# Kernel optimization log

Measured on AMD Instinct MI355X. Metric: run time of the kernel, lower is better.

## Reference

```python
import jax, jax.numpy as jnp
import numpy as np
from jax import lax

T, B, S = 64, 32, 64
V, E, H = 32000, 512, 512

def _p(key, shape, scale=0.05):
    return (jax.random.normal(key, shape, dtype=jnp.float32) * scale)

def setup_inputs() -> dict:
    key = jax.random.key(0)
    ks = jax.random.split(key, 24)
    inp = {
        'trg': jax.random.randint(ks[0], (T, B), 0, V),
        'encoded_src': jax.random.normal(ks[1], (S, B, 2 * H), dtype=jnp.float32),
        'emb': _p(ks[2], (V, E)),
        # LSTM layer 0: input = E + 2H
        'W_ih0': _p(ks[3], (4 * H, E + 2 * H)), 'W_hh0': _p(ks[4], (4 * H, H)),
        'b_ih0': _p(ks[5], (4 * H,)), 'b_hh0': _p(ks[6], (4 * H,)),
        # LSTM layer 1: input = H
        'W_ih1': _p(ks[7], (4 * H, H)), 'W_hh1': _p(ks[8], (4 * H, H)),
        'b_ih1': _p(ks[9], (4 * H,)), 'b_hh1': _p(ks[10], (4 * H,)),
        # attn_annot: 2H -> H
        'Wa': _p(ks[11], (H, 2 * H)), 'ba': _p(ks[12], (H,)),
        # attn_hidden: H -> H
        'Wh': _p(ks[13], (H, H)), 'bh': _p(ks[14], (H,)),
        # other: H -> 1
        'Wo': _p(ks[15], (1, H)), 'bo': _p(ks[16], (1,)),
        # penult: 3H -> E
        'Wp': _p(ks[17], (E, 3 * H)), 'bp': _p(ks[18], (E,)),
        # out bias (weight tied to emb)
        'b_out': _p(ks[19], (V,)),
    }
    return inp

def _lstm_cell(x, h, c, W_ih, W_hh, b_ih, b_hh):
    # PyTorch gate order: i, f, g, o
    g = x @ W_ih.T + b_ih + h @ W_hh.T + b_hh
    i, f, gg, o = jnp.split(g, 4, axis=-1)
    c_new = jax.nn.sigmoid(f) * c + jax.nn.sigmoid(i) * jnp.tanh(gg)
    h_new = jax.nn.sigmoid(o) * jnp.tanh(c_new)
    return h_new, c_new

def reference(trg, encoded_src, emb, W_ih0, W_hh0, b_ih0, b_hh0,
              W_ih1, W_hh1, b_ih1, b_hh1, Wa, ba, Wh, bh, Wo, bo,
              Wp, bp, b_out):
    trg_emb = emb[trg]                                # [T,B,E]
    annot_scores = encoded_src @ Wa.T + ba            # [S,B,H]
    Hd = W_hh0.shape[1]
    Bd = encoded_src.shape[1]
    h0 = jnp.zeros((2, Bd, Hd), dtype=encoded_src.dtype)
    c0 = jnp.zeros((2, Bd, Hd), dtype=encoded_src.dtype)
    ctx0 = jnp.zeros((Bd, encoded_src.shape[2]), dtype=encoded_src.dtype)

    def step(carry, emb_t):
        h, c, ctx = carry
        x = jnp.concatenate([emb_t, ctx], axis=1)      # [B, E+2H]
        h0n, c0n = _lstm_cell(x,   h[0], c[0], W_ih0, W_hh0, b_ih0, b_hh0)
        h1n, c1n = _lstm_cell(h0n, h[1], c[1], W_ih1, W_hh1, b_ih1, b_hh1)
        out = h1n                                      # [B,H]
        hs = out @ Wh.T + bh                           # [B,H]
        e = jnp.tanh(hs[None] + annot_scores) @ Wo.T + bo   # [S,B,1]
        a = jax.nn.softmax(e, axis=0)[..., 0]          # [S,B]
        ctx_new = jnp.einsum('sb,sbd->bd', a, encoded_src)  # [B,2H]
        stacked = jnp.concatenate([out, ctx_new], axis=1)   # [B,3H]
        return (jnp.stack([h0n, h1n]), jnp.stack([c0n, c1n]), ctx_new), stacked

    (h, c, _), all_scores = lax.scan(step, (h0, c0, ctx0), trg_emb)  # all_scores [T,B,3H]
    pen = all_scores @ Wp.T + bp                       # [T,B,E]
    logits = pen @ emb.T + b_out                       # [T,B,V] (tied weights)
    scores = jax.nn.log_softmax(logits, axis=2)
    return (scores, h, c)
```

## Files before the change

kernel.cpp:

```cpp
#include <hip/hip_runtime.h>


typedef unsigned short u16;
typedef short bf16x8 __attribute__((ext_vector_type(8)));
typedef float f32x4 __attribute__((ext_vector_type(4)));

#define MFMA_BF16(a, b, c) __builtin_amdgcn_mfma_f32_16x16x32_bf16((a), (b), (c), 0, 0, 0)

struct __attribute__((aligned(8))) U16x4 { u16 x, y, z, w; };

__device__ __forceinline__ float b2f(u16 u) {
  unsigned v = ((unsigned)u) << 16; float f; __builtin_memcpy(&f, &v, 4); return f;
}
__device__ __forceinline__ u16 f2b(float f) {
  unsigned u; __builtin_memcpy(&u, &f, 4);
  u = (u + 0x7FFFu + ((u >> 16) & 1u)) >> 16;
  return (u16)u;
}
__device__ __forceinline__ float sigm(float x) { return 1.f / (1.f + __expf(-x)); }
__device__ __forceinline__ float tanh_fast(float x) {
  x = fminf(fmaxf(x, -15.f), 15.f);
  float e = __expf(2.f * x);
  return (e - 1.f) / (e + 1.f);
}

__device__ __forceinline__ bf16x8 bl16(const u16* p) {
  bf16x8 v;
  asm volatile("global_load_dwordx4 %0, %1, off sc0 sc1" : "=v"(v) : "v"(p) : "memory");
  return v;
}
__device__ __forceinline__ float blf(const float* p) {
  float v;
  asm volatile("global_load_dword %0, %1, off sc0 sc1" : "=v"(v) : "v"(p) : "memory");
  return v;
}
__device__ __forceinline__ u16 blu16(const u16* p) {
  unsigned v;
  asm volatile("global_load_ushort %0, %1, off sc0 sc1" : "=v"(v) : "v"(p) : "memory");
  return (u16)v;
}
__device__ __forceinline__ void bs16(u16* p, u16 d) {
  unsigned dd = d;
  asm volatile("global_store_short %0, %1, off sc0 sc1" :: "v"(p), "v"(dd) : "memory");
}
__device__ __forceinline__ void bs32(float* p, float d) {
  asm volatile("global_store_dword %0, %1, off sc0 sc1" :: "v"(p), "v"(d) : "memory");
}
__device__ __forceinline__ void bs32u(u16* p, unsigned d) {
  asm volatile("global_store_dword %0, %1, off sc0 sc1" :: "v"(p), "v"(d) : "memory");
}
__device__ __forceinline__ void vmwait() {
  asm volatile("s_waitcnt vmcnt(0)" ::: "memory");
  __builtin_amdgcn_sched_barrier(0);
}

__global__ void f2b4_kernel(const float* __restrict__ src, u16* __restrict__ dst, long n4) {
  long i = (long)blockIdx.x * blockDim.x + threadIdx.x;
  long stride = (long)gridDim.x * blockDim.x;
  for (; i < n4; i += stride) {
    float4 v = ((const float4*)src)[i];
    U16x4 o; o.x = f2b(v.x); o.y = f2b(v.y); o.z = f2b(v.z); o.w = f2b(v.w);
    ((U16x4*)dst)[i] = o;
  }
}

__global__ void f2b4_strided(const float* __restrict__ src, u16* __restrict__ dst,
                             int rows, int cols4, int sld, int soff, int dld, int doff) {
  int total = rows * cols4;
  for (int i = blockIdx.x * blockDim.x + threadIdx.x; i < total; i += gridDim.x * blockDim.x) {
    int r = i / cols4, c4 = i - r * cols4;
    float4 v = *(const float4*)(src + (size_t)r * sld + soff + c4 * 4);
    U16x4 o; o.x = f2b(v.x); o.y = f2b(v.y); o.z = f2b(v.z); o.w = f2b(v.w);
    *(U16x4*)(dst + (size_t)r * dld + doff + c4 * 4) = o;
  }
}

__global__ void gather_emb_kernel(const int* __restrict__ trg, const float* __restrict__ emb,
                                  u16* __restrict__ out) {
  int r = blockIdx.x;
  int v = trg[r];
  const float* srow = emb + (size_t)v * 512;
  u16* drow = out + (size_t)r * 512;
  for (int e = threadIdx.x; e < 128; e += blockDim.x) {
    float4 x = ((const float4*)srow)[e];
    U16x4 o; o.x = f2b(x.x); o.y = f2b(x.y); o.z = f2b(x.z); o.w = f2b(x.w);
    ((U16x4*)drow)[e] = o;
  }
}

__global__ void annot_tr_kernel(const float* __restrict__ annot, u16* __restrict__ abt) {
  int b = blockIdx.x >> 6, s = blockIdx.x & 63;
  const float* src = annot + (size_t)(s * 32 + b) * 512;
  u16* dst = abt + (size_t)(b * 64 + s) * 512;
  int j = threadIdx.x;
  float4 v = ((const float4*)src)[j];
  U16x4 o; o.x = f2b(v.x); o.y = f2b(v.y); o.z = f2b(v.z); o.w = f2b(v.w);
  ((U16x4*)dst)[j] = o;
}

__global__ void enc_tr_kernel(const float* __restrict__ enc, u16* __restrict__ ebt) {
  int b = blockIdx.x >> 6, s = blockIdx.x & 63;
  const float* src = enc + (size_t)(s * 32 + b) * 1024;
  u16* dst = ebt + (size_t)(b * 64 + s) * 1024;
  int j = threadIdx.x;
  float4 v = ((const float4*)src)[j];
  U16x4 o; o.x = f2b(v.x); o.y = f2b(v.y); o.z = f2b(v.z); o.w = f2b(v.w);
  ((U16x4*)dst)[j] = o;
}

template <int MODE>
__global__ __launch_bounds__(256) void gemm_bt(
    const u16* __restrict__ A, const u16* __restrict__ B,
    float* __restrict__ outF, u16* __restrict__ outB,
    const float* __restrict__ bias0, const float* __restrict__ bias1,
    int N, int K, int ntiles, float* __restrict__ pmax, float* __restrict__ psum) {
  const int l = threadIdx.x & 63, wv = threadIdx.x >> 6;
  const int m0 = blockIdx.x * 128 + wv * 32;
  const int n0 = blockIdx.y * 64;
  const int kg = ((l >> 4) << 3);
  const u16* Ap0 = A + (size_t)(m0 + (l & 15)) * K + kg;
  const u16* Ap1 = Ap0 + (size_t)16 * K;
  const u16* Bp = B + (size_t)(n0 + (l & 15)) * K + kg;
  f32x4 acc[2][4] = {};
  for (int k0 = 0; k0 < K; k0 += 32) {
    bf16x8 a0 = *(const bf16x8*)(Ap0 + k0);
    bf16x8 a1 = *(const bf16x8*)(Ap1 + k0);
#pragma unroll
    for (int nf = 0; nf < 4; ++nf) {
      bf16x8 bb = *(const bf16x8*)(Bp + (size_t)(nf * 16) * K + k0);
      acc[0][nf] = MFMA_BF16(a0, bb, acc[0][nf]);
      acc[1][nf] = MFMA_BF16(a1, bb, acc[1][nf]);
    }
  }
  float biasv[4];
#pragma unroll
  for (int nf = 0; nf < 4; ++nf) {
    int col = n0 + nf * 16 + (l & 15);
    float bv = bias0 ? bias0[col] : 0.f;
    if (bias1) bv += bias1[col];
    biasv[nf] = bv;
  }
#pragma unroll
  for (int mi = 0; mi < 2; ++mi)
#pragma unroll
    for (int nf = 0; nf < 4; ++nf)
#pragma unroll
      for (int i = 0; i < 4; ++i) acc[mi][nf][i] += biasv[nf];

#pragma unroll
  for (int mi = 0; mi < 2; ++mi)
#pragma unroll
    for (int i = 0; i < 4; ++i) {
      int row = m0 + mi * 16 + ((l >> 4) << 2) + i;
#pragma unroll
      for (int nf = 0; nf < 4; ++nf) {
        int col = n0 + nf * 16 + (l & 15);
        if constexpr (MODE == 1)
          outB[(size_t)row * N + col] = f2b(acc[mi][nf][i]);
        else
          outF[(size_t)row * N + col] = acc[mi][nf][i];
      }
    }
  if constexpr (MODE == 2) {
    float lm[2][4], se[2][4];
#pragma unroll
    for (int mi = 0; mi < 2; ++mi)
#pragma unroll
      for (int i = 0; i < 4; ++i) {
        float m_ = acc[mi][0][i];
#pragma unroll
        for (int nf = 1; nf < 4; ++nf) m_ = fmaxf(m_, acc[mi][nf][i]);
        lm[mi][i] = m_;
      }
#pragma unroll
    for (int d = 1; d < 16; d <<= 1)
#pragma unroll
      for (int mi = 0; mi < 2; ++mi)
#pragma unroll
        for (int i = 0; i < 4; ++i) lm[mi][i] = fmaxf(lm[mi][i], __shfl_xor(lm[mi][i], d));
#pragma unroll
    for (int mi = 0; mi < 2; ++mi)
#pragma unroll
      for (int i = 0; i < 4; ++i) {
        float s_ = 0.f;
#pragma unroll
        for (int nf = 0; nf < 4; ++nf) s_ += __expf(acc[mi][nf][i] - lm[mi][i]);
        se[mi][i] = s_;
      }
#pragma unroll
    for (int d = 1; d < 16; d <<= 1)
#pragma unroll
      for (int mi = 0; mi < 2; ++mi)
#pragma unroll
        for (int i = 0; i < 4; ++i) se[mi][i] += __shfl_xor(se[mi][i], d);
    if ((l & 15) == 0) {
#pragma unroll
      for (int mi = 0; mi < 2; ++mi)
#pragma unroll
        for (int i = 0; i < 4; ++i) {
          int row = m0 + mi * 16 + ((l >> 4) << 2) + i;
          pmax[(size_t)row * ntiles + blockIdx.y] = lm[mi][i];
          psum[(size_t)row * ntiles + blockIdx.y] = se[mi][i];
        }
    }
  }
}

__device__ __forceinline__ void grid_barrier(unsigned* flags, unsigned phase) {
  __syncthreads();
  if (threadIdx.x == 0) {
    __hip_atomic_store(flags + blockIdx.x * 32, phase, __ATOMIC_RELAXED,
                       __HIP_MEMORY_SCOPE_AGENT);
  }
  if (threadIdx.x < 32) {
    int spins = 0;
    while (__hip_atomic_load(flags + threadIdx.x * 32, __ATOMIC_RELAXED,
                             __HIP_MEMORY_SCOPE_AGENT) < phase &&
           spins < 2000000) ++spins;
  }
  __syncthreads();
}

__global__ __launch_bounds__(512, 2) void scan_kernel(
    const u16* __restrict__ xW0,
    const u16* __restrict__ Wcat0,
    const u16* __restrict__ Wcat1,
    const u16* __restrict__ Whb,
    const float* __restrict__ b_ih1, const float* __restrict__ b_hh1,
    const float* __restrict__ bh, const float* __restrict__ Wo, const float* __restrict__ bo,
    const u16* __restrict__ annot_bt,
    const u16* __restrict__ enc_bt,
    u16* __restrict__ ctxb,
    u16* __restrict__ h0b,
    u16* __restrict__ h1b,
    float* __restrict__ c0, float* __restrict__ c1,
    float* __restrict__ hs,
    u16* __restrict__ scoresb,
    float* __restrict__ dout_hc,
    unsigned* __restrict__ flags) {
  __shared__ float sm[16384];
  const int w = blockIdx.x;
  const int tid = threadIdx.x;
  const int l = tid & 63, wv = tid >> 6;
  const int jh0 = w * 16;
  const int bE = tid >> 4, jlE = tid & 15;
  unsigned phase = 0;

  float gb1[4];
#pragma unroll
  for (int g = 0; g < 4; ++g) gb1[g] = b_ih1[g * 512 + jh0 + jlE] + b_hh1[g * 512 + jh0 + jlE];
  const float bhv = bh[jh0 + jlE];
  const float bov = bo[0];

  for (int t = 0; t < 64; ++t) {
    const int pA = t & 1;
    {
      const int kg = ((l >> 4) << 3);
      u16 xw[4];
      {
        const u16* xp = xW0 + (size_t)(t * 32 + bE) * 2048 + jh0 + jlE;
#pragma unroll
        for (int g = 0; g < 4; ++g) xw[g] = blu16(xp + g * 512);
      }
      bf16x8 a0[6], a1[6];
#pragma unroll
      for (int kk = 0; kk < 6; ++kk) {
        const int k0 = wv * 192 + kk * 32;
        const u16* ab; int ld, off;
        if (k0 < 1024) { ab = ctxb; ld = 1024; off = k0; }
        else { ab = h0b + pA * 32 * 512; ld = 512; off = k0 - 1024; }
        a0[kk] = bl16(ab + (size_t)(l & 15) * ld + off + kg);
        a1[kk] = bl16(ab + (size_t)((l & 15) + 16) * ld + off + kg);
      }
      vmwait();
      f32x4 acc[2][4] = {};
#pragma unroll
      for (int kk = 0; kk < 6; ++kk) {
        const int k0 = wv * 192 + kk * 32;
#pragma unroll
        for (int g = 0; g < 4; ++g) {
          bf16x8 bb = *(const bf16x8*)(Wcat0 + (size_t)(g * 512 + jh0 + (l & 15)) * 1536 + k0 + kg);
          acc[0][g] = MFMA_BF16(a0[kk], bb, acc[0][g]);
          acc[1][g] = MFMA_BF16(a1[kk], bb, acc[1][g]);
        }
      }
#pragma unroll
      for (int mi = 0; mi < 2; ++mi)
#pragma unroll
        for (int g = 0; g < 4; ++g)
#pragma unroll
          for (int i = 0; i < 4; ++i) {
            int m = mi * 16 + ((l >> 4) << 2) + i;
            sm[(wv * 32 + m) * 64 + g * 16 + (l & 15)] = acc[mi][g][i];
          }
      __syncthreads();
      {
        const int b = bE, jl = jlE, jh = jh0 + jl;
        float gate[4];
#pragma unroll
        for (int g = 0; g < 4; ++g) {
          float s = 0.f;
#pragma unroll
          for (int kv = 0; kv < 8; ++kv) s += sm[(kv * 32 + b) * 64 + g * 16 + jl];
          gate[g] = s + b2f(xw[g]);
        }
        float cn = sigm(gate[1]) * c0[b * 512 + jh] + sigm(gate[0]) * tanh_fast(gate[2]);
        float hn = sigm(gate[3]) * tanh_fast(cn);
        c0[b * 512 + jh] = cn;
        bs16(h0b + (pA ^ 1) * 32 * 512 + b * 512 + jh, f2b(hn));
        if (t == 63) { dout_hc[b * 512 + jh] = hn; dout_hc[32768 + b * 512 + jh] = cn; }
      }
    }
    grid_barrier(flags, ++phase);
    {
      const int kg = ((l >> 4) << 3);
      bf16x8 a0[4], a1[4];
#pragma unroll
      for (int kk = 0; kk < 4; ++kk) {
        const int k0 = wv * 128 + kk * 32;
        const u16* ab; int off;
        if (k0 < 512) { ab = h0b + (pA ^ 1) * 32 * 512; off = k0; }
        else { ab = h1b + pA * 32 * 512; off = k0 - 512; }
        a0[kk] = bl16(ab + (size_t)(l & 15) * 512 + off + kg);
        a1[kk] = bl16(ab + (size_t)((l & 15) + 16) * 512 + off + kg);
      }
      vmwait();
      f32x4 acc[2][4] = {};
#pragma unroll
      for (int kk = 0; kk < 4; ++kk) {
        const int k0 = wv * 128 + kk * 32;
#pragma unroll
        for (int g = 0; g < 4; ++g) {
          bf16x8 bb = *(const bf16x8*)(Wcat1 + (size_t)(g * 512 + jh0 + (l & 15)) * 1024 + k0 + kg);
          acc[0][g] = MFMA_BF16(a0[kk], bb, acc[0][g]);
          acc[1][g] = MFMA_BF16(a1[kk], bb, acc[1][g]);
        }
      }
#pragma unroll
      for (int mi = 0; mi < 2; ++mi)
#pragma unroll
        for (int g = 0; g < 4; ++g)
#pragma unroll
          for (int i = 0; i < 4; ++i) {
            int m = mi * 16 + ((l >> 4) << 2) + i;
            sm[(wv * 32 + m) * 64 + g * 16 + (l & 15)] = acc[mi][g][i];
          }
      __syncthreads();
      {
        const int b = bE, jl = jlE, jh = jh0 + jl;
        float gate[4];
#pragma unroll
        for (int g = 0; g < 4; ++g) {
          float s = 0.f;
#pragma unroll
          for (int kv = 0; kv < 8; ++kv) s += sm[(kv * 32 + b) * 64 + g * 16 + jl];
          gate[g] = s + gb1[g];
        }
        float cn = sigm(gate[1]) * c1[b * 512 + jh] + sigm(gate[0]) * tanh_fast(gate[2]);
        float hn = sigm(gate[3]) * tanh_fast(cn);
        c1[b * 512 + jh] = cn;
        u16 hb = f2b(hn);
        bs16(h1b + (pA ^ 1) * 32 * 512 + b * 512 + jh, hb);
        bs16(scoresb + (size_t)(t * 32 + b) * 1536 + jh, hb);
        if (t == 63) { dout_hc[16384 + b * 512 + jh] = hn; dout_hc[32768 + 16384 + b * 512 + jh] = cn; }
      }
    }
    grid_barrier(flags, ++phase);
    {
      const int kg = ((l >> 4) << 3);
      const u16* h1n = h1b + (pA ^ 1) * 32 * 512;
      bf16x8 a0[2], a1[2];
#pragma unroll
      for (int kk = 0; kk < 2; ++kk) {
        const int k0 = wv * 64 + kk * 32;
        a0[kk] = bl16(h1n + (size_t)(l & 15) * 512 + k0 + kg);
        a1[kk] = bl16(h1n + (size_t)((l & 15) + 16) * 512 + k0 + kg);
      }
      vmwait();
      f32x4 acc2[2] = {};
#pragma unroll
      for (int kk = 0; kk < 2; ++kk) {
        const int k0 = wv * 64 + kk * 32;
        bf16x8 bb = *(const bf16x8*)(Whb + (size_t)(jh0 + (l & 15)) * 512 + k0 + kg);
        acc2[0] = MFMA_BF16(a0[kk], bb, acc2[0]);
        acc2[1] = MFMA_BF16(a1[kk], bb, acc2[1]);
      }
#pragma unroll
      for (int mi = 0; mi < 2; ++mi)
#pragma unroll
        for (int i = 0; i < 4; ++i)
          sm[(wv * 32 + mi * 16 + ((l >> 4) << 2) + i) * 16 + (l & 15)] = acc2[mi][i];
      __syncthreads();
      {
        const int b = bE, jl = jlE;
        float s = 0.f;
#pragma unroll
        for (int kv = 0; kv < 8; ++kv) s += sm[(kv * 32 + b) * 16 + jl];
        bs32(hs + b * 512 + jh0 + jl, s + bhv);
      }
    }
    grid_barrier(flags, ++phase);
    {
      const int b = w;
      float* hs_s = sm;
      float* wo_s = sm + 512;
      float* red = sm + 1024;
      float* a_s = sm + 1536;
      float hv = blf(hs + b * 512 + tid);
      float wov = Wo[tid];
      vmwait();
      hs_s[tid] = hv;
      wo_s[tid] = wov;
      __syncthreads();
      const int s_ = tid >> 3, ks = tid & 7;
      const u16* arow = annot_bt + (size_t)(b * 64 + s_) * 512 + ks * 64;
      float accv = 0.f;
#pragma unroll
      for (int kk8 = 0; kk8 < 8; ++kk8) {
        bf16x8 av = *(const bf16x8*)(arow + kk8 * 8);
#pragma unroll
        for (int j = 0; j < 8; ++j) {
          int k = ks * 64 + kk8 * 8 + j;
          accv += tanh_fast(hs_s[k] + b2f((u16)av[j])) * wo_s[k];
        }
      }
      red[tid] = accv;
      __syncthreads();
      if (tid < 64) {
        float e = bov;
#pragma unroll
        for (int j = 0; j < 8; ++j) e += red[tid * 8 + j];
        float mx = e;
#pragma unroll
        for (int d = 1; d < 64; d <<= 1) mx = fmaxf(mx, __shfl_xor(mx, d));
        float p = __expf(e - mx);
        float ss = p;
#pragma unroll
        for (int d = 1; d < 64; d <<= 1) ss += __shfl_xor(ss, d);
        a_s[tid] = p / ss;
      }
      __syncthreads();
      float cx0 = 0.f, cx1 = 0.f;
      const u16* erow = enc_bt + (size_t)b * 65536 + tid * 2;
#pragma unroll 8
      for (int s2 = 0; s2 < 64; ++s2) {
        unsigned ev = *(const unsigned*)(erow + (size_t)s2 * 1024);
        float av = a_s[s2];
        cx0 += av * b2f((u16)(ev & 0xFFFFu));
        cx1 += av * b2f((u16)(ev >> 16));
      }
      u16 u0 = f2b(cx0), u1 = f2b(cx1);
      unsigned pk = (unsigned)u0 | ((unsigned)u1 << 16);
      bs32u(ctxb + b * 1024 + tid * 2, pk);
      bs32u(scoresb + (size_t)(t * 32 + b) * 1536 + 512 + tid * 2, pk);
    }
    grid_barrier(flags, ++phase);
  }
}

__global__ __launch_bounds__(256) void lse_kernel(const float* __restrict__ pmax,
                                                  const float* __restrict__ psum,
                                                  float* __restrict__ lse, int nt) {
  __shared__ float red[256];
  const int r = blockIdx.x;
  float m = -3.4e38f;
  for (int j = threadIdx.x; j < nt; j += 256) m = fmaxf(m, pmax[(size_t)r * nt + j]);
  red[threadIdx.x] = m; __syncthreads();
  for (int s = 128; s > 0; s >>= 1) {
    if (threadIdx.x < s) red[threadIdx.x] = fmaxf(red[threadIdx.x], red[threadIdx.x + s]);
    __syncthreads();
  }
  const float M = red[0]; __syncthreads();
  float s_ = 0.f;
  for (int j = threadIdx.x; j < nt; j += 256)
    s_ += psum[(size_t)r * nt + j] * __expf(pmax[(size_t)r * nt + j] - M);
  red[threadIdx.x] = s_; __syncthreads();
  for (int s = 128; s > 0; s >>= 1) {
    if (threadIdx.x < s) red[threadIdx.x] += red[threadIdx.x + s];
    __syncthreads();
  }
  if (threadIdx.x == 0) lse[r] = M + logf(red[0]);
}

__global__ void finalize_kernel(float* __restrict__ out, const float* __restrict__ lse) {
  const long n4 = 16384000;
  for (long i = (long)blockIdx.x * blockDim.x + threadIdx.x; i < n4;
       i += (long)gridDim.x * blockDim.x) {
    float4 v = ((float4*)out)[i];
    float L = lse[i / 8000];
    v.x -= L; v.y -= L; v.z -= L; v.w -= L;
    ((float4*)out)[i] = v;
  }
}

extern "C" void kernel_launch(void* const* d_in, const int* in_sizes, int n_in,
                              void* d_out, int out_size, void* d_ws, size_t ws_size,
                              hipStream_t stream) {
  const int* trg = (const int*)d_in[0];
  const float* enc = (const float*)d_in[1];
  const float* emb = (const float*)d_in[2];
  const float* W_ih0 = (const float*)d_in[3];
  const float* W_hh0 = (const float*)d_in[4];
  const float* b_ih0 = (const float*)d_in[5];
  const float* b_hh0 = (const float*)d_in[6];
  const float* W_ih1 = (const float*)d_in[7];
  const float* W_hh1 = (const float*)d_in[8];
  const float* b_ih1 = (const float*)d_in[9];
  const float* b_hh1 = (const float*)d_in[10];
  const float* Wa = (const float*)d_in[11];
  const float* ba = (const float*)d_in[12];
  const float* Wh = (const float*)d_in[13];
  const float* bh = (const float*)d_in[14];
  const float* Wo = (const float*)d_in[15];
  const float* bo = (const float*)d_in[16];
  const float* Wp = (const float*)d_in[17];
  const float* bp = (const float*)d_in[18];
  const float* b_out = (const float*)d_in[19];
  float* out = (float*)d_out;

  unsigned char* ws = (unsigned char*)d_ws;
  size_t off = 0;
  auto alloc = [&](size_t bytes) -> void* {
    void* p = ws + off; off += (bytes + 255) & ~(size_t)255; return p;
  };
  u16* emb_b = (u16*)alloc(32768000);
  u16* trgemb_b = (u16*)alloc(2097152);
  u16* enc_b = (u16*)alloc(4194304);
  u16* Wemb0_b = (u16*)alloc(2097152);
  u16* Wcat0_b = (u16*)alloc(6291456);
  u16* Wcat1_b = (u16*)alloc(4194304);
  u16* Wa_b = (u16*)alloc(1048576);
  u16* Wh_b = (u16*)alloc(524288);
  u16* Wp_b = (u16*)alloc(1572864);
  u16* xW0_b = (u16*)alloc(8388608);
  float* annot = (float*)alloc(4194304);
  u16* scoresb = (u16*)alloc(6291456);
  u16* pen_b = (u16*)alloc(2097152);
  u16* ctxb = (u16*)alloc(65536);
  u16* h0b = (u16*)alloc(65536);
  u16* h1b = (u16*)alloc(65536);
  float* c0 = (float*)alloc(65536);
  float* c1 = (float*)alloc(65536);
  float* hsbuf = (float*)alloc(65536);
  float* pmax = (float*)alloc(4194304);
  float* psum = (float*)alloc(4194304);
  float* lse = (float*)alloc(8192);
  unsigned* flags = (unsigned*)alloc(4096);
  if (off > ws_size) return;

  u16* annot_bt = (u16*)pmax;
  u16* enc_bt = (u16*)psum;

  hipMemsetAsync(ctxb, 0, 65536, stream);
  hipMemsetAsync(h0b, 0, 65536, stream);
  hipMemsetAsync(h1b, 0, 65536, stream);
  hipMemsetAsync(c0, 0, 65536, stream);
  hipMemsetAsync(c1, 0, 65536, stream);
  hipMemsetAsync(flags, 0, 4096, stream);

  f2b4_kernel<<<1024, 256, 0, stream>>>(emb, emb_b, 4096000);
  f2b4_kernel<<<256, 256, 0, stream>>>(enc, enc_b, 524288);
  f2b4_kernel<<<128, 256, 0, stream>>>(Wa, Wa_b, 131072);
  f2b4_kernel<<<64, 256, 0, stream>>>(Wh, Wh_b, 65536);
  f2b4_kernel<<<128, 256, 0, stream>>>(Wp, Wp_b, 196608);
  f2b4_strided<<<512, 256, 0, stream>>>(W_ih0, Wemb0_b, 2048, 128, 1536, 0, 512, 0);
  f2b4_strided<<<512, 256, 0, stream>>>(W_ih0, Wcat0_b, 2048, 256, 1536, 512, 1536, 0);
  f2b4_strided<<<512, 256, 0, stream>>>(W_hh0, Wcat0_b, 2048, 128, 512, 0, 1536, 1024);
  f2b4_strided<<<512, 256, 0, stream>>>(W_ih1, Wcat1_b, 2048, 128, 512, 0, 1024, 0);
  f2b4_strided<<<512, 256, 0, stream>>>(W_hh1, Wcat1_b, 2048, 128, 512, 0, 1024, 512);
  gather_emb_kernel<<<2048, 128, 0, stream>>>(trg, emb, trgemb_b);
  enc_tr_kernel<<<2048, 256, 0, stream>>>(enc, enc_bt);

  gemm_bt<1><<<dim3(16, 32), 256, 0, stream>>>(trgemb_b, Wemb0_b, nullptr, xW0_b,
                                               b_ih0, b_hh0, 2048, 512, 0, nullptr, nullptr);
  gemm_bt<0><<<dim3(16, 8), 256, 0, stream>>>(enc_b, Wa_b, annot, nullptr,
                                              ba, nullptr, 512, 1024, 0, nullptr, nullptr);
  annot_tr_kernel<<<2048, 128, 0, stream>>>(annot, annot_bt);

  scan_kernel<<<32, 512, 0, stream>>>(xW0_b, Wcat0_b, Wcat1_b, Wh_b, b_ih1, b_hh1, bh, Wo, bo,
                                      annot_bt, enc_bt, ctxb, h0b, h1b, c0, c1, hsbuf, scoresb,
                                      out + 65536000, flags);
  gemm_bt<1><<<dim3(16, 8), 256, 0, stream>>>(scoresb, Wp_b, nullptr, pen_b,
                                              bp, nullptr, 512, 1536, 0, nullptr, nullptr);
  gemm_bt<2><<<dim3(16, 500), 256, 0, stream>>>(pen_b, emb_b, out, nullptr,
                                                b_out, nullptr, 32000, 512, 500, pmax, psum);
  lse_kernel<<<2048, 256, 0, stream>>>(pmax, psum, lse, 500);
  finalize_kernel<<<2048, 256, 0, stream>>>(out, lse);
}
```

Baseline: 2.522 ms.

## Overlap output projection and vocab GEMM with recurrent scan in a persistent mega-kernel

Merges the recurrent scan, the penultimate projection and the vocabulary logits GEMM into one persistent 224-block kernel. Every 7th block runs the serial LSTM/attention recurrence, and the remaining 192 blocks wait on the step flags and compute pen and logits for timestep t while the recurrence moves ahead. This hides the large tied-weight GEMM behind the latency-bound scan. In exchange it adds spin-waiting on flags, relies on all blocks being co-resident, and changes the vocab tile width and the partial max/sum layout to 250 tiles.

```diff
diff --git a/kernel.cpp b/kernel.cpp
--- a/kernel.cpp
+++ b/kernel.cpp
@@ -43,10 +43,10 @@
   unsigned dd = d;
   asm volatile("global_store_short %0, %1, off sc0 sc1" :: "v"(p), "v"(dd) : "memory");
 }
-__device__ __forceinline__ void bs32(float* p, float d) {
+__device__ __forceinline__ void bs32u(u16* p, unsigned d) {
   asm volatile("global_store_dword %0, %1, off sc0 sc1" :: "v"(p), "v"(d) : "memory");
 }
-__device__ __forceinline__ void bs32u(u16* p, unsigned d) {
+__device__ __forceinline__ void bsf32(float* p, float d) {
   asm volatile("global_store_dword %0, %1, off sc0 sc1" :: "v"(p), "v"(d) : "memory");
 }
 __device__ __forceinline__ void vmwait() {
@@ -113,7 +113,7 @@
     const u16* __restrict__ A, const u16* __restrict__ B,
     float* __restrict__ outF, u16* __restrict__ outB,
     const float* __restrict__ bias0, const float* __restrict__ bias1,
-    int N, int K, int ntiles, float* __restrict__ pmax, float* __restrict__ psum) {
+    int N, int K) {
   const int l = threadIdx.x & 63, wv = threadIdx.x >> 6;
   const int m0 = blockIdx.x * 128 + wv * 32;
   const int n0 = blockIdx.y * 64;
@@ -143,85 +143,36 @@
 #pragma unroll
   for (int mi = 0; mi < 2; ++mi)
 #pragma unroll
-    for (int nf = 0; nf < 4; ++nf)
-#pragma unroll
-      for (int i = 0; i < 4; ++i) acc[mi][nf][i] += biasv[nf];
-
-#pragma unroll
-  for (int mi = 0; mi < 2; ++mi)
-#pragma unroll
     for (int i = 0; i < 4; ++i) {
       int row = m0 + mi * 16 + ((l >> 4) << 2) + i;
 #pragma unroll
       for (int nf = 0; nf < 4; ++nf) {
         int col = n0 + nf * 16 + (l & 15);
+        float v = acc[mi][nf][i] + biasv[nf];
         if constexpr (MODE == 1)
-          outB[(size_t)row * N + col] = f2b(acc[mi][nf][i]);
+          outB[(size_t)row * N + col] = f2b(v);
         else
-          outF[(size_t)row * N + col] = acc[mi][nf][i];
+          outF[(size_t)row * N + col] = v;
       }
     }
-  if constexpr (MODE == 2) {
-    float lm[2][4], se[2][4];
-#pragma unroll
-    for (int mi = 0; mi < 2; ++mi)
-#pragma unroll
-      for (int i = 0; i < 4; ++i) {
-        float m_ = acc[mi][0][i];
-#pragma unroll
-        for (int nf = 1; nf < 4; ++nf) m_ = fmaxf(m_, acc[mi][nf][i]);
-        lm[mi][i] = m_;
-      }
-#pragma unroll
-    for (int d = 1; d < 16; d <<= 1)
-#pragma unroll
-      for (int mi = 0; mi < 2; ++mi)
-#pragma unroll
-        for (int i = 0; i < 4; ++i) lm[mi][i] = fmaxf(lm[mi][i], __shfl_xor(lm[mi][i], d));
-#pragma unroll
-    for (int mi = 0; mi < 2; ++mi)
-#pragma unroll
-      for (int i = 0; i < 4; ++i) {
-        float s_ = 0.f;
-#pragma unroll
-        for (int nf = 0; nf < 4; ++nf) s_ += __expf(acc[mi][nf][i] - lm[mi][i]);
-        se[mi][i] = s_;
-      }
-#pragma unroll
-    for (int d = 1; d < 16; d <<= 1)
-#pragma unroll
-      for (int mi = 0; mi < 2; ++mi)
-#pragma unroll
-        for (int i = 0; i < 4; ++i) se[mi][i] += __shfl_xor(se[mi][i], d);
-    if ((l & 15) == 0) {
-#pragma unroll
-      for (int mi = 0; mi < 2; ++mi)
-#pragma unroll
-        for (int i = 0; i < 4; ++i) {
-          int row = m0 + mi * 16 + ((l >> 4) << 2) + i;
-          pmax[(size_t)row * ntiles + blockIdx.y] = lm[mi][i];
-          psum[(size_t)row * ntiles + blockIdx.y] = se[mi][i];
-        }
-    }
-  }
-}
-
-__device__ __forceinline__ void grid_barrier(unsigned* flags, unsigned phase) {
+}
+
+__device__ __forceinline__ void grid_barrier(unsigned* flags, unsigned phase, int w) {
   __syncthreads();
   if (threadIdx.x == 0) {
-    __hip_atomic_store(flags + blockIdx.x * 32, phase, __ATOMIC_RELAXED,
+    __hip_atomic_store(flags + (size_t)w * 32, phase, __ATOMIC_RELAXED,
                        __HIP_MEMORY_SCOPE_AGENT);
   }
   if (threadIdx.x < 32) {
     int spins = 0;
-    while (__hip_atomic_load(flags + threadIdx.x * 32, __ATOMIC_RELAXED,
+    while (__hip_atomic_load(flags + (size_t)threadIdx.x * 32, __ATOMIC_RELAXED,
                              __HIP_MEMORY_SCOPE_AGENT) < phase &&
            spins < 2000000) ++spins;
   }
   __syncthreads();
 }
 
-__global__ __launch_bounds__(512, 2) void scan_kernel(
+__global__ __launch_bounds__(512, 2) void mega_kernel(
     const u16* __restrict__ xW0,
     const u16* __restrict__ Wcat0,
     const u16* __restrict__ Wcat1,
@@ -230,231 +181,375 @@
     const float* __restrict__ bh, const float* __restrict__ Wo, const float* __restrict__ bo,
     const u16* __restrict__ annot_bt,
     const u16* __restrict__ enc_bt,
-    u16* __restrict__ ctxb,
-    u16* __restrict__ h0b,
-    u16* __restrict__ h1b,
-    float* __restrict__ c0, float* __restrict__ c1,
-    float* __restrict__ hs,
-    u16* __restrict__ scoresb,
-    float* __restrict__ dout_hc,
-    unsigned* __restrict__ flags) {
+    u16* ctxb, u16* h0b, u16* h1b,
+    float* c0, float* c1,
+    float* hs,
+    u16* scoresb,
+    float* dout_hc,
+    unsigned* flags,
+    const u16* __restrict__ Wp,
+    const float* __restrict__ bp, const u16* __restrict__ emb_b,
+    const float* __restrict__ b_out,
+    u16* pen_b,
+    float* out, float* pmax, float* psum) {
   __shared__ float sm[16384];
-  const int w = blockIdx.x;
+  const int bx = blockIdx.x;
   const int tid = threadIdx.x;
   const int l = tid & 63, wv = tid >> 6;
-  const int jh0 = w * 16;
-  const int bE = tid >> 4, jlE = tid & 15;
-  unsigned phase = 0;
-
-  float gb1[4];
-#pragma unroll
-  for (int g = 0; g < 4; ++g) gb1[g] = b_ih1[g * 512 + jh0 + jlE] + b_hh1[g * 512 + jh0 + jlE];
-  const float bhv = bh[jh0 + jlE];
-  const float bov = bo[0];
-
-  for (int t = 0; t < 64; ++t) {
-    const int pA = t & 1;
-    {
-      const int kg = ((l >> 4) << 3);
-      u16 xw[4];
+
+  if (bx % 7 == 0) {
+    const int w = bx / 7;
+    const int jh0 = w * 16;
+    const int bE = tid >> 4, jlE = tid & 15;
+    unsigned phase = 0;
+
+    float gb1[4];
+#pragma unroll
+    for (int g = 0; g < 4; ++g) gb1[g] = b_ih1[g * 512 + jh0 + jlE] + b_hh1[g * 512 + jh0 + jlE];
+    const float bhv = bh[jh0 + jlE];
+    const float bov = bo[0];
+
+    for (int t = 0; t < 64; ++t) {
+      const int pA = t & 1;
       {
-        const u16* xp = xW0 + (size_t)(t * 32 + bE) * 2048 + jh0 + jlE;
-#pragma unroll
-        for (int g = 0; g < 4; ++g) xw[g] = blu16(xp + g * 512);
-      }
-      bf16x8 a0[6], a1[6];
-#pragma unroll
-      for (int kk = 0; kk < 6; ++kk) {
-        const int k0 = wv * 192 + kk * 32;
-        const u16* ab; int ld, off;
-        if (k0 < 1024) { ab = ctxb; ld = 1024; off = k0; }
-        else { ab = h0b + pA * 32 * 512; ld = 512; off = k0 - 1024; }
-        a0[kk] = bl16(ab + (size_t)(l & 15) * ld + off + kg);
-        a1[kk] = bl16(ab + (size_t)((l & 15) + 16) * ld + off + kg);
-      }
-      vmwait();
-      f32x4 acc[2][4] = {};
-#pragma unroll
-      for (int kk = 0; kk < 6; ++kk) {
-        const int k0 = wv * 192 + kk * 32;
-#pragma unroll
-        for (int g = 0; g < 4; ++g) {
-          bf16x8 bb = *(const bf16x8*)(Wcat0 + (size_t)(g * 512 + jh0 + (l & 15)) * 1536 + k0 + kg);
-          acc[0][g] = MFMA_BF16(a0[kk], bb, acc[0][g]);
-          acc[1][g] = MFMA_BF16(a1[kk], bb, acc[1][g]);
-        }
-      }
-#pragma unroll
-      for (int mi = 0; mi < 2; ++mi)
-#pragma unroll
-        for (int g = 0; g < 4; ++g)
+        const int kg = ((l >> 4) << 3);
+        u16 xw[4];
+        {
+          const u16* xp = xW0 + (size_t)(t * 32 + bE) * 2048 + jh0 + jlE;
+#pragma unroll
+          for (int g = 0; g < 4; ++g) xw[g] = blu16(xp + g * 512);
+        }
+        bf16x8 a0[6], a1[6];
+#pragma unroll
+        for (int kk = 0; kk < 6; ++kk) {
+          const int k0 = wv * 192 + kk * 32;
+          const u16* ab; int ld, off;
+          if (k0 < 1024) { ab = ctxb; ld = 1024; off = k0; }
+          else { ab = h0b + pA * 16384; ld = 512; off = k0 - 1024; }
+          a0[kk] = bl16(ab + (size_t)(l & 15) * ld + off + kg);
+          a1[kk] = bl16(ab + (size_t)((l & 15) + 16) * ld + off + kg);
+        }
+        vmwait();
+        f32x4 acc[2][4] = {};
+#pragma unroll
+        for (int kk = 0; kk < 6; ++kk) {
+          const int k0 = wv * 192 + kk * 32;
+#pragma unroll
+          for (int g = 0; g < 4; ++g) {
+            bf16x8 bb = *(const bf16x8*)(Wcat0 + (size_t)(g * 512 + jh0 + (l & 15)) * 1536 + k0 + kg);
+            acc[0][g] = MFMA_BF16(a0[kk], bb, acc[0][g]);
+            acc[1][g] = MFMA_BF16(a1[kk], bb, acc[1][g]);
+          }
+        }
+#pragma unroll
+        for (int mi = 0; mi < 2; ++mi)
+#pragma unroll
+          for (int g = 0; g < 4; ++g)
+#pragma unroll
+            for (int i = 0; i < 4; ++i) {
+              int m = mi * 16 + ((l >> 4) << 2) + i;
+              sm[(wv * 32 + m) * 64 + g * 16 + (l & 15)] = acc[mi][g][i];
+            }
+        __syncthreads();
+        {
+          const int b = bE, jl = jlE, jh = jh0 + jl;
+          float gate[4];
+#pragma unroll
+          for (int g = 0; g < 4; ++g) {
+            float s = 0.f;
+#pragma unroll
+            for (int kv = 0; kv < 8; ++kv) s += sm[(kv * 32 + b) * 64 + g * 16 + jl];
+            gate[g] = s + b2f(xw[g]);
+          }
+          float cn = sigm(gate[1]) * c0[b * 512 + jh] + sigm(gate[0]) * tanh_fast(gate[2]);
+          float hn = sigm(gate[3]) * tanh_fast(cn);
+          c0[b * 512 + jh] = cn;
+          bs16(h0b + (pA ^ 1) * 16384 + b * 512 + jh, f2b(hn));
+          if (t == 63) { dout_hc[b * 512 + jh] = hn; dout_hc[32768 + b * 512 + jh] = cn; }
+        }
+      }
+      grid_barrier(flags, ++phase, w);
+      {
+        const int kg = ((l >> 4) << 3);
+        bf16x8 a0[4], a1[4];
+#pragma unroll
+        for (int kk = 0; kk < 4; ++kk) {
+          const int k0 = wv * 128 + kk * 32;
+          const u16* ab; int off;
+          if (k0 < 512) { ab = h0b + (pA ^ 1) * 16384; off = k0; }
+          else { ab = h1b + pA * 16384; off = k0 - 512; }
+          a0[kk] = bl16(ab + (size_t)(l & 15) * 512 + off + kg);
+          a1[kk] = bl16(ab + (size_t)((l & 15) + 16) * 512 + off + kg);
+        }
+        vmwait();
+        f32x4 acc[2][4] = {};
+#pragma unroll
+        for (int kk = 0; kk < 4; ++kk) {
+          const int k0 = wv * 128 + kk * 32;
+#pragma unroll
+          for (int g = 0; g < 4; ++g) {
+            bf16x8 bb = *(const bf16x8*)(Wcat1 + (size_t)(g * 512 + jh0 + (l & 15)) * 1024 + k0 + kg);
+            acc[0][g] = MFMA_BF16(a0[kk], bb, acc[0][g]);
+            acc[1][g] = MFMA_BF16(a1[kk], bb, acc[1][g]);
+          }
+        }
+#pragma unroll
+        for (int mi = 0; mi < 2; ++mi)
+#pragma unroll
+          for (int g = 0; g < 4; ++g)
+#pragma unroll
+            for (int i = 0; i < 4; ++i) {
+              int m = mi * 16 + ((l >> 4) << 2) + i;
+              sm[(wv * 32 + m) * 64 + g * 16 + (l & 15)] = acc[mi][g][i];
+            }
+        __syncthreads();
+        {
+          const int b = bE, jl = jlE, jh = jh0 + jl;
+          float gate[4];
+#pragma unroll
+          for (int g = 0; g < 4; ++g) {
+            float s = 0.f;
+#pragma unroll
+            for (int kv = 0; kv < 8; ++kv) s += sm[(kv * 32 + b) * 64 + g * 16 + jl];
+            gate[g] = s + gb1[g];
+          }
+          float cn = sigm(gate[1]) * c1[b * 512 + jh] + sigm(gate[0]) * tanh_fast(gate[2]);
+          float hn = sigm(gate[3]) * tanh_fast(cn);
+          c1[b * 512 + jh] = cn;
+          u16 hb = f2b(hn);
+          bs16(h1b + (pA ^ 1) * 16384 + b * 512 + jh, hb);
+          bs16(scoresb + (size_t)(t * 32 + b) * 1536 + jh, hb);
+          if (t == 63) { dout_hc[16384 + b * 512 + jh] = hn; dout_hc[49152 + b * 512 + jh] = cn; }
+        }
+      }
+      grid_barrier(flags, ++phase, w);
+      {
+        const int kg = ((l >> 4) << 3);
+        const u16* h1n = h1b + (pA ^ 1) * 16384;
+        bf16x8 a0[2], a1[2];
+#pragma unroll
+        for (int kk = 0; kk < 2; ++kk) {
+          const int k0 = wv * 64 + kk * 32;
+          a0[kk] = bl16(h1n + (size_t)(l & 15) * 512 + k0 + kg);
+          a1[kk] = bl16(h1n + (size_t)((l & 15) + 16) * 512 + k0 + kg);
+        }
+        vmwait();
+        f32x4 acc2[2] = {};
+#pragma unroll
+        for (int kk = 0; kk < 2; ++kk) {
+          const int k0 = wv * 64 + kk * 32;
+          bf16x8 bb = *(const bf16x8*)(Whb + (size_t)(jh0 + (l & 15)) * 512 + k0 + kg);
+          acc2[0] = MFMA_BF16(a0[kk], bb, acc2[0]);
+          acc2[1] = MFMA_BF16(a1[kk], bb, acc2[1]);
+        }
+#pragma unroll
+        for (int mi = 0; mi < 2; ++mi)
+#pragma unroll
+          for (int i = 0; i < 4; ++i)
+            sm[(wv * 32 + mi * 16 + ((l >> 4) << 2) + i) * 16 + (l & 15)] = acc2[mi][i];
+        __syncthreads();
+        {
+          const int b = bE, jl = jlE;
+          float s = 0.f;
+#pragma unroll
+          for (int kv = 0; kv < 8; ++kv) s += sm[(kv * 32 + b) * 16 + jl];
+          bsf32(hs + b * 512 + jh0 + jl, s + bhv);
+        }
+      }
+      grid_barrier(flags, ++phase, w);
+      {
+        const int b = w;
+        float* hs_s = sm;
+        float* wo_s = sm + 512;
+        float* red = sm + 1024;
+        float* a_s = sm + 1536;
+        float hv = blf(hs + b * 512 + tid);
+        float wov = Wo[tid];
+        vmwait();
+        hs_s[tid] = hv;
+        wo_s[tid] = wov;
+        __syncthreads();
+        const int s_ = tid >> 3, ks = tid & 7;
+        const u16* arow = annot_bt + (size_t)(b * 64 + s_) * 512 + ks * 64;
+        float accv = 0.f;
+#pragma unroll
+        for (int kk8 = 0; kk8 < 8; ++kk8) {
+          bf16x8 av = *(const bf16x8*)(arow + kk8 * 8);
+#pragma unroll
+          for (int j = 0; j < 8; ++j) {
+            int k = ks * 64 + kk8 * 8 + j;
+            accv += tanh_fast(hs_s[k] + b2f((u16)av[j])) * wo_s[k];
+          }
+        }
+        red[tid] = accv;
+        __syncthreads();
+        if (tid < 64) {
+          float e = bov;
+#pragma unroll
+          for (int j = 0; j < 8; ++j) e += red[tid * 8 + j];
+          float mx = e;
+#pragma unroll
+          for (int d = 1; d < 64; d <<= 1) mx = fmaxf(mx, __shfl_xor(mx, d));
+          float p = __expf(e - mx);
+          float ss = p;
+#pragma unroll
+          for (int d = 1; d < 64; d <<= 1) ss += __shfl_xor(ss, d);
+          a_s[tid] = p / ss;
+        }
+        __syncthreads();
+        float cx0 = 0.f, cx1 = 0.f;
+        const u16* erow = enc_bt + (size_t)b * 65536 + tid * 2;
+#pragma unroll 8
+        for (int s2 = 0; s2 < 64; ++s2) {
+          unsigned ev = *(const unsigned*)(erow + (size_t)s2 * 1024);
+          float av = a_s[s2];
+          cx0 += av * b2f((u16)(ev & 0xFFFFu));
+          cx1 += av * b2f((u16)(ev >> 16));
+        }
+        unsigned pk = (unsigned)f2b(cx0) | ((unsigned)f2b(cx1) << 16);
+        bs32u(ctxb + b * 1024 + tid * 2, pk);
+        bs32u(scoresb + (size_t)(t * 32 + b) * 1536 + 512 + tid * 2, pk);
+      }
+      grid_barrier(flags, ++phase, w);
+    }
+  } else {
+    const int wid = bx - bx / 7 - 1;
+    const int kg = (l >> 4) << 3;
+    const int tile1 = wid, tile2 = 192 + wid;
+    const int ntile = (tile2 < 250) ? 2 : 1;
+
+    for (int t = 0; t < 64; ++t) {
+      if (tid < 32) {
+        int spins = 0;
+        while (__hip_atomic_load(flags + (size_t)tid * 32, __ATOMIC_RELAXED,
+                                 __HIP_MEMORY_SCOPE_AGENT) < (unsigned)(4 * (t + 1)) &&
+               spins < 8000000) { __builtin_amdgcn_s_sleep(2); ++spins; }
+      }
+      __syncthreads();
+
+      if (wid == (t % 192)) {
+        const u16* Ap0 = scoresb + (size_t)(t * 32 + (l & 15)) * 1536 + kg;
+        const u16* Ap1 = Ap0 + (size_t)16 * 1536;
+        const int cv = wv * 64;
+        const u16* Bp = Wp + (size_t)(cv + (l & 15)) * 1536 + kg;
+        f32x4 acc[2][4] = {};
+        for (int kc = 0; kc < 1536; kc += 128) {
+          bf16x8 bfr[4][4];
+#pragma unroll
+          for (int kk = 0; kk < 4; ++kk)
+#pragma unroll
+            for (int nf = 0; nf < 4; ++nf)
+              bfr[kk][nf] = bl16(Bp + (size_t)(nf * 16) * 1536 + kc + kk * 32);
+          vmwait();
+#pragma unroll
+          for (int kk = 0; kk < 4; ++kk) {
+            bf16x8 a0 = *(const bf16x8*)(Ap0 + kc + kk * 32);
+            bf16x8 a1 = *(const bf16x8*)(Ap1 + kc + kk * 32);
+#pragma unroll
+            for (int nf = 0; nf < 4; ++nf) {
+              acc[0][nf] = MFMA_BF16(a0, bfr[kk][nf], acc[0][nf]);
+              acc[1][nf] = MFMA_BF16(a1, bfr[kk][nf], acc[1][nf]);
+            }
+          }
+        }
+#pragma unroll
+        for (int mi = 0; mi < 2; ++mi)
 #pragma unroll
           for (int i = 0; i < 4; ++i) {
-            int m = mi * 16 + ((l >> 4) << 2) + i;
-            sm[(wv * 32 + m) * 64 + g * 16 + (l & 15)] = acc[mi][g][i];
-          }
+            int row = t * 32 + mi * 16 + ((l >> 4) << 2) + i;
+#pragma unroll
+            for (int nf = 0; nf < 4; ++nf) {
+              int col = cv + nf * 16 + (l & 15);
+              bs16(pen_b + (size_t)row * 512 + col, f2b(acc[mi][nf][i] + bp[col]));
+            }
+          }
+        vmwait();
+        __syncthreads();
+        if (tid == 0)
+          __hip_atomic_store(flags + 2048 + t, 1u, __ATOMIC_RELAXED,
+                             __HIP_MEMORY_SCOPE_AGENT);
+      }
+      if (tid == 0) {
+        int spins = 0;
+        while (__hip_atomic_load(flags + 2048 + t, __ATOMIC_RELAXED,
+                                 __HIP_MEMORY_SCOPE_AGENT) == 0 &&
+               spins < 8000000) { __builtin_amdgcn_s_sleep(2); ++spins; }
+      }
       __syncthreads();
-      {
-        const int b = bE, jl = jlE, jh = jh0 + jl;
-        float gate[4];
-#pragma unroll
-        for (int g = 0; g < 4; ++g) {
+
+      const u16* Ap0 = pen_b + (size_t)(t * 32 + (l & 15)) * 512 + kg;
+      const u16* Ap1 = Ap0 + (size_t)16 * 512;
+      for (int ti = 0; ti < ntile; ++ti) {
+        const int tile = (ti == 0) ? tile1 : tile2;
+        const int colb = tile * 128 + wv * 16;
+        const u16* Bp = emb_b + (size_t)(colb + (l & 15)) * 512 + kg;
+        f32x4 acc[2] = {};
+        for (int kc = 0; kc < 512; kc += 256) {
+          bf16x8 bfr[8];
+#pragma unroll
+          for (int kk = 0; kk < 8; ++kk) bfr[kk] = bl16(Bp + kc + kk * 32);
+          vmwait();
+#pragma unroll
+          for (int kk = 0; kk < 8; ++kk) {
+            bf16x8 a0 = *(const bf16x8*)(Ap0 + kc + kk * 32);
+            bf16x8 a1 = *(const bf16x8*)(Ap1 + kc + kk * 32);
+            acc[0] = MFMA_BF16(a0, bfr[kk], acc[0]);
+            acc[1] = MFMA_BF16(a1, bfr[kk], acc[1]);
+          }
+        }
+        const float bov = b_out[colb + (l & 15)];
+        float lm[2][4], se[2][4];
+#pragma unroll
+        for (int mi = 0; mi < 2; ++mi)
+#pragma unroll
+          for (int i = 0; i < 4; ++i) {
+            float v = acc[mi][i] + bov;
+            acc[mi][i] = v;
+            int row = t * 32 + mi * 16 + ((l >> 4) << 2) + i;
+            bsf32(out + (size_t)row * 32000 + colb + (l & 15), v);
+            lm[mi][i] = v;
+          }
+#pragma unroll
+        for (int d = 1; d < 16; d <<= 1)
+#pragma unroll
+          for (int mi = 0; mi < 2; ++mi)
+#pragma unroll
+            for (int i = 0; i < 4; ++i) lm[mi][i] = fmaxf(lm[mi][i], __shfl_xor(lm[mi][i], d));
+#pragma unroll
+        for (int mi = 0; mi < 2; ++mi)
+#pragma unroll
+          for (int i = 0; i < 4; ++i) se[mi][i] = __expf(acc[mi][i] - lm[mi][i]);
+#pragma unroll
+        for (int d = 1; d < 16; d <<= 1)
+#pragma unroll
+          for (int mi = 0; mi < 2; ++mi)
+#pragma unroll
+            for (int i = 0; i < 4; ++i) se[mi][i] += __shfl_xor(se[mi][i], d);
+        __syncthreads();
+        if ((l & 15) == 0) {
+#pragma unroll
+          for (int mi = 0; mi < 2; ++mi)
+#pragma unroll
+            for (int i = 0; i < 4; ++i) {
+              int rowl = mi * 16 + ((l >> 4) << 2) + i;
+              sm[rowl * 8 + wv] = lm[mi][i];
+              sm[256 + rowl * 8 + wv] = se[mi][i];
+            }
+        }
+        __syncthreads();
+        if (tid < 32) {
+          float m = -3.4e38f;
+#pragma unroll
+          for (int j = 0; j < 8; ++j) m = fmaxf(m, sm[tid * 8 + j]);
           float s = 0.f;
 #pragma unroll
-          for (int kv = 0; kv < 8; ++kv) s += sm[(kv * 32 + b) * 64 + g * 16 + jl];
-          gate[g] = s + b2f(xw[g]);
-        }
-        float cn = sigm(gate[1]) * c0[b * 512 + jh] + sigm(gate[0]) * tanh_fast(gate[2]);
-        float hn = sigm(gate[3]) * tanh_fast(cn);
-        c0[b * 512 + jh] = cn;
-        bs16(h0b + (pA ^ 1) * 32 * 512 + b * 512 + jh, f2b(hn));
-        if (t == 63) { dout_hc[b * 512 + jh] = hn; dout_hc[32768 + b * 512 + jh] = cn; }
+          for (int j = 0; j < 8; ++j) s += sm[256 + tid * 8 + j] * __expf(sm[tid * 8 + j] - m);
+          bsf32(pmax + (size_t)(t * 32 + tid) * 250 + tile, m);
+          bsf32(psum + (size_t)(t * 32 + tid) * 250 + tile, s);
+        }
+        __syncthreads();
       }
     }
-    grid_barrier(flags, ++phase);
-    {
-      const int kg = ((l >> 4) << 3);
-      bf16x8 a0[4], a1[4];
-#pragma unroll
-      for (int kk = 0; kk < 4; ++kk) {
-        const int k0 = wv * 128 + kk * 32;
-        const u16* ab; int off;
-        if (k0 < 512) { ab = h0b + (pA ^ 1) * 32 * 512; off = k0; }
-        else { ab = h1b + pA * 32 * 512; off = k0 - 512; }
-        a0[kk] = bl16(ab + (size_t)(l & 15) * 512 + off + kg);
-        a1[kk] = bl16(ab + (size_t)((l & 15) + 16) * 512 + off + kg);
-      }
-      vmwait();
-      f32x4 acc[2][4] = {};
-#pragma unroll
-      for (int kk = 0; kk < 4; ++kk) {
-        const int k0 = wv * 128 + kk * 32;
-#pragma unroll
-        for (int g = 0; g < 4; ++g) {
-          bf16x8 bb = *(const bf16x8*)(Wcat1 + (size_t)(g * 512 + jh0 + (l & 15)) * 1024 + k0 + kg);
-          acc[0][g] = MFMA_BF16(a0[kk], bb, acc[0][g]);
-          acc[1][g] = MFMA_BF16(a1[kk], bb, acc[1][g]);
-        }
-      }
-#pragma unroll
-      for (int mi = 0; mi < 2; ++mi)
-#pragma unroll
-        for (int g = 0; g < 4; ++g)
-#pragma unroll
-          for (int i = 0; i < 4; ++i) {
-            int m = mi * 16 + ((l >> 4) << 2) + i;
-            sm[(wv * 32 + m) * 64 + g * 16 + (l & 15)] = acc[mi][g][i];
-          }
-      __syncthreads();
-      {
-        const int b = bE, jl = jlE, jh = jh0 + jl;
-        float gate[4];
-#pragma unroll
-        for (int g = 0; g < 4; ++g) {
-          float s = 0.f;
-#pragma unroll
-          for (int kv = 0; kv < 8; ++kv) s += sm[(kv * 32 + b) * 64 + g * 16 + jl];
-          gate[g] = s + gb1[g];
-        }
-        float cn = sigm(gate[1]) * c1[b * 512 + jh] + sigm(gate[0]) * tanh_fast(gate[2]);
-        float hn = sigm(gate[3]) * tanh_fast(cn);
-        c1[b * 512 + jh] = cn;
-        u16 hb = f2b(hn);
-        bs16(h1b + (pA ^ 1) * 32 * 512 + b * 512 + jh, hb);
-        bs16(scoresb + (size_t)(t * 32 + b) * 1536 + jh, hb);
-        if (t == 63) { dout_hc[16384 + b * 512 + jh] = hn; dout_hc[32768 + 16384 + b * 512 + jh] = cn; }
-      }
-    }
-    grid_barrier(flags, ++phase);
-    {
-      const int kg = ((l >> 4) << 3);
-      const u16* h1n = h1b + (pA ^ 1) * 32 * 512;
-      bf16x8 a0[2], a1[2];
-#pragma unroll
-      for (int kk = 0; kk < 2; ++kk) {
-        const int k0 = wv * 64 + kk * 32;
-        a0[kk] = bl16(h1n + (size_t)(l & 15) * 512 + k0 + kg);
-        a1[kk] = bl16(h1n + (size_t)((l & 15) + 16) * 512 + k0 + kg);
-      }
-      vmwait();
-      f32x4 acc2[2] = {};
-#pragma unroll
-      for (int kk = 0; kk < 2; ++kk) {
-        const int k0 = wv * 64 + kk * 32;
-        bf16x8 bb = *(const bf16x8*)(Whb + (size_t)(jh0 + (l & 15)) * 512 + k0 + kg);
-        acc2[0] = MFMA_BF16(a0[kk], bb, acc2[0]);
-        acc2[1] = MFMA_BF16(a1[kk], bb, acc2[1]);
-      }
-#pragma unroll
-      for (int mi = 0; mi < 2; ++mi)
-#pragma unroll
-        for (int i = 0; i < 4; ++i)
-          sm[(wv * 32 + mi * 16 + ((l >> 4) << 2) + i) * 16 + (l & 15)] = acc2[mi][i];
-      __syncthreads();
-      {
-        const int b = bE, jl = jlE;
-        float s = 0.f;
-#pragma unroll
-        for (int kv = 0; kv < 8; ++kv) s += sm[(kv * 32 + b) * 16 + jl];
-        bs32(hs + b * 512 + jh0 + jl, s + bhv);
-      }
-    }
-    grid_barrier(flags, ++phase);
-    {
-      const int b = w;
-      float* hs_s = sm;
-      float* wo_s = sm + 512;
-      float* red = sm + 1024;
-      float* a_s = sm + 1536;
-      float hv = blf(hs + b * 512 + tid);
-      float wov = Wo[tid];
-      vmwait();
-      hs_s[tid] = hv;
-      wo_s[tid] = wov;
-      __syncthreads();
-      const int s_ = tid >> 3, ks = tid & 7;
-      const u16* arow = annot_bt + (size_t)(b * 64 + s_) * 512 + ks * 64;
-      float accv = 0.f;
-#pragma unroll
-      for (int kk8 = 0; kk8 < 8; ++kk8) {
-        bf16x8 av = *(const bf16x8*)(arow + kk8 * 8);
-#pragma unroll
-        for (int j = 0; j < 8; ++j) {
-          int k = ks * 64 + kk8 * 8 + j;
-          accv += tanh_fast(hs_s[k] + b2f((u16)av[j])) * wo_s[k];
-        }
-      }
-      red[tid] = accv;
-      __syncthreads();
-      if (tid < 64) {
-        float e = bov;
-#pragma unroll
-        for (int j = 0; j < 8; ++j) e += red[tid * 8 + j];
-        float mx = e;
-#pragma unroll
-        for (int d = 1; d < 64; d <<= 1) mx = fmaxf(mx, __shfl_xor(mx, d));
-        float p = __expf(e - mx);
-        float ss = p;
-#pragma unroll
-        for (int d = 1; d < 64; d <<= 1) ss += __shfl_xor(ss, d);
-        a_s[tid] = p / ss;
-      }
-      __syncthreads();
-      float cx0 = 0.f, cx1 = 0.f;
-      const u16* erow = enc_bt + (size_t)b * 65536 + tid * 2;
-#pragma unroll 8
-      for (int s2 = 0; s2 < 64; ++s2) {
-        unsigned ev = *(const unsigned*)(erow + (size_t)s2 * 1024);
-        float av = a_s[s2];
-        cx0 += av * b2f((u16)(ev & 0xFFFFu));
-        cx1 += av * b2f((u16)(ev >> 16));
-      }
-      u16 u0 = f2b(cx0), u1 = f2b(cx1);
-      unsigned pk = (unsigned)u0 | ((unsigned)u1 << 16);
-      bs32u(ctxb + b * 1024 + tid * 2, pk);
-      bs32u(scoresb + (size_t)(t * 32 + b) * 1536 + 512 + tid * 2, pk);
-    }
-    grid_barrier(flags, ++phase);
   }
 }
 
@@ -536,30 +631,30 @@
   float* annot = (float*)alloc(4194304);
   u16* scoresb = (u16*)alloc(6291456);
   u16* pen_b = (u16*)alloc(2097152);
+  u16* annot_bt = (u16*)alloc(2097152);
+  u16* enc_bt = (u16*)alloc(4194304);
   u16* ctxb = (u16*)alloc(65536);
   u16* h0b = (u16*)alloc(65536);
   u16* h1b = (u16*)alloc(65536);
   float* c0 = (float*)alloc(65536);
   float* c1 = (float*)alloc(65536);
   float* hsbuf = (float*)alloc(65536);
-  float* pmax = (float*)alloc(4194304);
-  float* psum = (float*)alloc(4194304);
   float* lse = (float*)alloc(8192);
-  unsigned* flags = (unsigned*)alloc(4096);
+  unsigned* flags = (unsigned*)alloc(16384);
   if (off > ws_size) return;
 
-  u16* annot_bt = (u16*)pmax;
-  u16* enc_bt = (u16*)psum;
+  float* pmax = annot;
+  float* psum = (float*)enc_b;
 
   hipMemsetAsync(ctxb, 0, 65536, stream);
   hipMemsetAsync(h0b, 0, 65536, stream);
   hipMemsetAsync(h1b, 0, 65536, stream);
   hipMemsetAsync(c0, 0, 65536, stream);
   hipMemsetAsync(c1, 0, 65536, stream);
-  hipMemsetAsync(flags, 0, 4096, stream);
+  hipMemsetAsync(flags, 0, 16384, stream);
 
   f2b4_kernel<<<1024, 256, 0, stream>>>(emb, emb_b, 4096000);
-  f2b4_kernel<<<256, 256, 0, stream>>>(enc, enc_b, 524288);
+  f2b4_kernel<<<256, 256, 0, stream>>>(enc, (u16*)enc_b, 524288);
   f2b4_kernel<<<128, 256, 0, stream>>>(Wa, Wa_b, 131072);
   f2b4_kernel<<<64, 256, 0, stream>>>(Wh, Wh_b, 65536);
   f2b4_kernel<<<128, 256, 0, stream>>>(Wp, Wp_b, 196608);
@@ -572,18 +667,17 @@
   enc_tr_kernel<<<2048, 256, 0, stream>>>(enc, enc_bt);
 
   gemm_bt<1><<<dim3(16, 32), 256, 0, stream>>>(trgemb_b, Wemb0_b, nullptr, xW0_b,
-                                               b_ih0, b_hh0, 2048, 512, 0, nullptr, nullptr);
+                                               b_ih0, b_hh0, 2048, 512);
   gemm_bt<0><<<dim3(16, 8), 256, 0, stream>>>(enc_b, Wa_b, annot, nullptr,
-                                              ba, nullptr, 512, 1024, 0, nullptr, nullptr);
+                                              ba, nullptr, 512, 1024);
   annot_tr_kernel<<<2048, 128, 0, stream>>>(annot, annot_bt);
 
-  scan_kernel<<<32, 512, 0, stream>>>(xW0_b, Wcat0_b, Wcat1_b, Wh_b, b_ih1, b_hh1, bh, Wo, bo,
-                                      annot_bt, enc_bt, ctxb, h0b, h1b, c0, c1, hsbuf, scoresb,
-                                      out + 65536000, flags);
-  gemm_bt<1><<<dim3(16, 8), 256, 0, stream>>>(scoresb, Wp_b, nullptr, pen_b,
-                                              bp, nullptr, 512, 1536, 0, nullptr, nullptr);
-  gemm_bt<2><<<dim3(16, 500), 256, 0, stream>>>(pen_b, emb_b, out, nullptr,
-                                                b_out, nullptr, 32000, 512, 500, pmax, psum);
-  lse_kernel<<<2048, 256, 0, stream>>>(pmax, psum, lse, 500);
+  mega_kernel<<<224, 512, 0, stream>>>(
+      xW0_b, Wcat0_b, Wcat1_b, Wh_b, b_ih1, b_hh1, bh, Wo, bo,
+      annot_bt, enc_bt, ctxb, h0b, h1b, c0, c1, hsbuf, scoresb,
+      out + 65536000, flags,
+      Wp_b, bp, emb_b, b_out, pen_b, out, pmax, psum);
+
+  lse_kernel<<<2048, 256, 0, stream>>>(pmax, psum, lse, 250);
   finalize_kernel<<<2048, 256, 0, stream>>>(out, lse);
 }
```

Measured after the change: 9.714 ms. 285% more time.
